# Optimization experiments

Hardware: AMD Instinct MI355X
Metric: run time of the kernel (lower is better)

The kernel has to match this reference:

```python
import jax, jax.numpy as jnp
import numpy as np

RADIUS = 8
EPS = 0.0001


def box_filter_1d(x, axis, r):
    # cumsum summed-area trick; zero padding at edges (matches torch version)
    cs = jnp.swapaxes(jnp.cumsum(x, axis=axis), axis, 0)
    out = jnp.concatenate([
        cs[r:2 * r + 1],
        cs[2 * r + 1:] - cs[:-2 * r - 1],
        cs[-1:] - cs[-2 * r - 1:-r - 1],
    ], axis=0)
    return jnp.swapaxes(out, 0, axis)


def box_filter(x, r):
    for ax in range(2, x.ndim):
        x = box_filter_1d(x, ax, r)
    return x


def setup_inputs() -> dict:
    key = jax.random.key(0)
    k1, k2 = jax.random.split(key)
    I = jax.random.normal(k1, (8, 4, 768, 768), dtype=jnp.float32)
    p = jax.random.uniform(k2, (8, 1, 768, 768), dtype=jnp.float32)
    return {"I": I, "p": p}


def reference(I, p):
    r = RADIUS
    bs, c, h, w = I.shape
    f = lambda t: box_filter(t, r)

    N = f(jnp.ones_like(I[:, :1]))              # (b,1,h,w) window pixel counts
    I_mean = f(I) / N                            # (b,c,h,w)
    p_mean = f(p) / N                            # (b,1,h,w)
    Ip_mean = f(p * I) / N                       # (b,c,h,w)
    first_term = Ip_mean - p_mean * I_mean       # (b,c,h,w)

    # per-pixel cxc covariance of the guide
    cov = jnp.einsum('bchw,bdhw->bcdhw', I, I).reshape(bs, c * c, h, w)
    cov = (f(cov) / N).reshape(bs, c, c, h, w).transpose(0, 3, 4, 1, 2)  # (b,h,w,c,c)
    eps_mat = EPS * jnp.eye(c, dtype=I.dtype)
    second_term = jnp.linalg.inv(cov + eps_mat)  # batched small-matrix inverse

    # NOTE: einsum strings reproduce the original module exactly
    A = jnp.einsum('bchw,bhwcd->bchw', first_term, second_term)
    b = p_mean - jnp.einsum('bchw,bdhw->bhw', A, I_mean)[:, None]  # (b,1,h,w)

    A_mean = f(A) / N
    b_mean = f(b) / N
    q = jnp.einsum('bchw,bdhw->bhw', A_mean, I)[:, None] + b_mean
    return q
```

## Files before the change

### kernel.cpp

```cpp
#include <hip/hip_runtime.h>


#define HH 768
#define WW 768
#define CC 4
#define BB 8
#define RR 8
#define EPSF 1.0e-4f

#define TA 128
#define OUTA 112
#define SHA 24
#define NSTRIPE (HH / SHA)
#define NBAND 7

__device__ __forceinline__ void loadpix(const float* __restrict__ Ib,
                                        const float* __restrict__ pb,
                                        int row, int gc, float pr[19]) {
  const int off = row * WW + gc;
  const int chs = HH * WW;
  float i0 = Ib[off];
  float i1 = Ib[chs + off];
  float i2 = Ib[2 * chs + off];
  float i3 = Ib[3 * chs + off];
  float pv = pb[off];
  pr[0] = i0; pr[1] = i1; pr[2] = i2; pr[3] = i3;
  pr[4] = pv;
  pr[5] = pv * i0; pr[6] = pv * i1; pr[7] = pv * i2; pr[8] = pv * i3;
  pr[9]  = i0 * i0; pr[10] = i0 * i1; pr[11] = i0 * i2; pr[12] = i0 * i3;
  pr[13] = i1 * i1; pr[14] = i1 * i2; pr[15] = i1 * i3;
  pr[16] = i2 * i2; pr[17] = i2 * i3;
  pr[18] = i3 * i3;
}

__global__ __launch_bounds__(TA) void gf_stageA(const float* __restrict__ I,
                                                const float* __restrict__ p,
                                                float2* __restrict__ AB,
                                                float* __restrict__ sumI_ws,
                                                int storeSum) {
  __shared__ float v[TA][20];
  __shared__ float s4[TA][20];
  const int tid = threadIdx.x;
  const int band0 = (int)blockIdx.x * OUTA;
  const int r0 = (int)blockIdx.y * SHA;
  const int batch = (int)blockIdx.z;
  const int gc = band0 - RR + tid;
  const bool colok = (gc >= 0 && gc < WW);

  const float* Ib = I + (size_t)batch * CC * HH * WW;
  const float* pb = p + (size_t)batch * HH * WW;
  float* sIb = sumI_ws + (size_t)batch * HH * WW;

  float s[20];
#pragma unroll
  for (int k = 0; k < 20; ++k) s[k] = 0.0f;

  if (colok) {
    int rlo = r0 - RR - 1; if (rlo < 0) rlo = 0;
    for (int row = rlo; row < r0 + RR; ++row) {
      float pr[19]; loadpix(Ib, pb, row, gc, pr);
#pragma unroll
      for (int k = 0; k < 19; ++k) s[k] += pr[k];
      if (storeSum && r0 == 0)
        sIb[row * WW + gc] = pr[0] + pr[1] + pr[2] + pr[3];
    }
  }

  const int oc = band0 + tid;
  const bool outok = (tid < OUTA) && (oc < WW);
  const int nw = min(oc + RR, WW - 1) - max(oc - RR, 0) + 1;

  for (int r = r0; r < r0 + SHA; ++r) {
    if (colok) {
      int rl = r + RR;
      if (rl < HH) {
        float pr[19]; loadpix(Ib, pb, rl, gc, pr);
#pragma unroll
        for (int k = 0; k < 19; ++k) s[k] += pr[k];
        if (storeSum)
          sIb[rl * WW + gc] = pr[0] + pr[1] + pr[2] + pr[3];
      }
      int rt = r - RR - 1;
      if (rt >= 0) {
        float pr[19]; loadpix(Ib, pb, rt, gc, pr);
#pragma unroll
        for (int k = 0; k < 19; ++k) s[k] -= pr[k];
      }
    }
    {
      float4* vp = (float4*)(&v[tid][0]);
      vp[0] = make_float4(s[0],  s[1],  s[2],  s[3]);
      vp[1] = make_float4(s[4],  s[5],  s[6],  s[7]);
      vp[2] = make_float4(s[8],  s[9],  s[10], s[11]);
      vp[3] = make_float4(s[12], s[13], s[14], s[15]);
      vp[4] = make_float4(s[16], s[17], s[18], 0.0f);
    }
    __syncthreads();
    float t4[20];
    if (tid < TA - 3) {
      const float* a1 = &v[tid + 1][0];
      const float* a2 = &v[tid + 2][0];
      const float* a3 = &v[tid + 3][0];
      float4* op = (float4*)(&s4[tid][0]);
#pragma unroll
      for (int j = 0; j < 5; ++j) {
        float4 xa = ((const float4*)a1)[j];
        float4 xb = ((const float4*)a2)[j];
        float4 xc = ((const float4*)a3)[j];
        float o0 = s[4*j + 0] + xa.x + xb.x + xc.x;
        float o1 = s[4*j + 1] + xa.y + xb.y + xc.y;
        float o2 = s[4*j + 2] + xa.z + xb.z + xc.z;
        float o3 = s[4*j + 3] + xa.w + xb.w + xc.w;
        op[j] = make_float4(o0, o1, o2, o3);
        t4[4*j + 0] = o0; t4[4*j + 1] = o1; t4[4*j + 2] = o2; t4[4*j + 3] = o3;
      }
    }
    __syncthreads();
    if (outok) {
      float h[20];
      const float* q4  = &s4[tid + 4][0];
      const float* q8  = &s4[tid + 8][0];
      const float* q12 = &s4[tid + 12][0];
      const float* q16 = &v[tid + 16][0];
#pragma unroll
      for (int j = 0; j < 5; ++j) {
        float4 a4 = ((const float4*)q4)[j];
        float4 b4 = ((const float4*)q8)[j];
        float4 c4 = ((const float4*)q12)[j];
        float4 d4 = ((const float4*)q16)[j];
        h[4*j + 0] = t4[4*j + 0] + a4.x + b4.x + c4.x + d4.x;
        h[4*j + 1] = t4[4*j + 1] + a4.y + b4.y + c4.y + d4.y;
        h[4*j + 2] = t4[4*j + 2] + a4.z + b4.z + c4.z + d4.z;
        h[4*j + 3] = t4[4*j + 3] + a4.w + b4.w + c4.w + d4.w;
      }
      const int nh = min(r + RR, HH - 1) - max(r - RR, 0) + 1;
      const float invN = 1.0f / (float)(nh * nw);
      float Im0 = h[0] * invN, Im1 = h[1] * invN, Im2 = h[2] * invN, Im3 = h[3] * invN;
      float pm = h[4] * invN;
      float ft0 = h[5] * invN - pm * Im0;
      float ft1 = h[6] * invN - pm * Im1;
      float ft2 = h[7] * invN - pm * Im2;
      float ft3 = h[8] * invN - pm * Im3;
      float m[4][4];
      m[0][0] = h[9]  * invN + EPSF;
      m[0][1] = h[10] * invN;
      m[0][2] = h[11] * invN;
      m[0][3] = h[12] * invN;
      m[1][1] = h[13] * invN + EPSF;
      m[1][2] = h[14] * invN;
      m[1][3] = h[15] * invN;
      m[2][2] = h[16] * invN + EPSF;
      m[2][3] = h[17] * invN;
      m[3][3] = h[18] * invN + EPSF;
      m[1][0] = m[0][1]; m[2][0] = m[0][2]; m[3][0] = m[0][3];
      m[2][1] = m[1][2]; m[3][1] = m[1][3]; m[3][2] = m[2][3];
      float y[4] = {1.0f, 1.0f, 1.0f, 1.0f};
#pragma unroll
      for (int k = 0; k < 4; ++k) {
        float piv = 1.0f / m[k][k];
#pragma unroll
        for (int j = 0; j < 4; ++j) m[k][j] *= piv;
        y[k] *= piv;
#pragma unroll
        for (int i = 0; i < 4; ++i) {
          if (i == k) continue;
          float f = m[i][k];
#pragma unroll
          for (int j = 0; j < 4; ++j) m[i][j] -= f * m[k][j];
          y[i] -= f * y[k];
        }
      }
      float Asum = ft0 * y[0] + ft1 * y[1] + ft2 * y[2] + ft3 * y[3];
      float bv = pm - Asum * (Im0 + Im1 + Im2 + Im3);
      AB[((size_t)batch * HH + r) * WW + oc] = make_float2(Asum, bv);
    }
    __syncthreads();
  }
}

__global__ __launch_bounds__(TA) void gf_stageB(const float* __restrict__ I,
                                                const float2* __restrict__ AB,
                                                const float* __restrict__ sumI_ws,
                                                float* __restrict__ q, int useSum) {
  __shared__ float2 v2[TA];
  __shared__ float2 s42[TA];
  const int tid = threadIdx.x;
  const int band0 = (int)blockIdx.x * OUTA;
  const int r0 = (int)blockIdx.y * SHA;
  const int batch = (int)blockIdx.z;
  const int gc = band0 - RR + tid;
  const bool colok = (gc >= 0 && gc < WW);

  const float2* ABb = AB + (size_t)batch * HH * WW;
  const float* sIb = sumI_ws + (size_t)batch * HH * WW;
  const float* Ib = I + (size_t)batch * CC * HH * WW;

  float sA = 0.0f, sB = 0.0f;
  if (colok) {
    int rlo = r0 - RR - 1; if (rlo < 0) rlo = 0;
    for (int row = rlo; row < r0 + RR; ++row) {
      float2 t = ABb[row * WW + gc];
      sA += t.x; sB += t.y;
    }
  }
  const int oc = band0 + tid;
  const bool outok = (tid < OUTA) && (oc < WW);
  const int nw = min(oc + RR, WW - 1) - max(oc - RR, 0) + 1;

  for (int r = r0; r < r0 + SHA; ++r) {
    if (colok) {
      int rl = r + RR;
      if (rl < HH) { float2 t = ABb[rl * WW + gc]; sA += t.x; sB += t.y; }
      int rt = r - RR - 1;
      if (rt >= 0) { float2 t = ABb[rt * WW + gc]; sA -= t.x; sB -= t.y; }
    }
    v2[tid] = make_float2(sA, sB);
    __syncthreads();
    float tx = 0.0f, ty = 0.0f;
    if (tid < TA - 3) {
      float2 a = v2[tid + 1], b = v2[tid + 2], c = v2[tid + 3];
      tx = sA + a.x + b.x + c.x;
      ty = sB + a.y + b.y + c.y;
      s42[tid] = make_float2(tx, ty);
    }
    __syncthreads();
    if (outok) {
      float2 a = s42[tid + 4], b = s42[tid + 8], c = s42[tid + 12], d = v2[tid + 16];
      float hA = tx + a.x + b.x + c.x + d.x;
      float hB = ty + a.y + b.y + c.y + d.y;
      const int nh = min(r + RR, HH - 1) - max(r - RR, 0) + 1;
      const float invN = 1.0f / (float)(nh * nw);
      const int off = r * WW + oc;
      float sumI;
      if (useSum) {
        sumI = sIb[off];
      } else {
        const int chs = HH * WW;
        sumI = Ib[off] + Ib[chs + off] + Ib[2 * chs + off] + Ib[3 * chs + off];
      }
      q[((size_t)batch * HH + r) * WW + oc] = (hA * sumI + hB) * invN;
    }
    __syncthreads();
  }
}

extern "C" void kernel_launch(void* const* d_in, const int* in_sizes, int n_in,
                              void* d_out, int out_size, void* d_ws, size_t ws_size,
                              hipStream_t stream) {
  const float* I = (const float*)d_in[0];
  const float* p = (const float*)d_in[1];
  float* q = (float*)d_out;

  const size_t npix = (size_t)BB * HH * WW;
  float2* AB = (float2*)d_ws;
  float* sumI_ws = (float*)(AB + npix);
  const size_t need = npix * sizeof(float2) + npix * sizeof(float);
  const int useSum = (ws_size >= need) ? 1 : 0;

  dim3 grid(NBAND, NSTRIPE, BB);
  dim3 block(TA);
  hipLaunchKernelGGL(gf_stageA, grid, block, 0, stream, I, p, AB, sumI_ws, useSum);
  hipLaunchKernelGGL(gf_stageB, grid, block, 0, stream, I, AB, sumI_ws, q, useSum);
}
```

Baseline: 235.6 us.

## Prefetch next rows in stage A and preload sliding window in stage B

Stage A now loads the raw 5 values for the next entering and leaving rows one iteration ahead (software pipelining), computing the 19 products from registers so global latency overlaps the solve. Its stripe height drops from 24 to 16 rows, giving more blocks but more halo recomputation. Stage B, which keeps its own 24-row stripe, loads the whole 41-row window of A/b values and the sumI values into registers up front, removing dependent loads from the per-row loop. This raises register pressure and may reduce occupancy.

```diff
diff --git a/kernel.cpp b/kernel.cpp
--- a/kernel.cpp
+++ b/kernel.cpp
@@ -10,27 +10,33 @@
 
 #define TA 128
 #define OUTA 112
-#define SHA 24
+#define SHA 16
 #define NSTRIPE (HH / SHA)
 #define NBAND 7
 
-__device__ __forceinline__ void loadpix(const float* __restrict__ Ib,
-                                        const float* __restrict__ pb,
-                                        int row, int gc, float pr[19]) {
+#define SHB 24
+#define NSTRIPEB (HH / SHB)
+
+__device__ __forceinline__ void load5(const float* __restrict__ Ib,
+                                      const float* __restrict__ pb,
+                                      int row, int gc, float o[5]) {
   const int off = row * WW + gc;
   const int chs = HH * WW;
-  float i0 = Ib[off];
-  float i1 = Ib[chs + off];
-  float i2 = Ib[2 * chs + off];
-  float i3 = Ib[3 * chs + off];
-  float pv = pb[off];
-  pr[0] = i0; pr[1] = i1; pr[2] = i2; pr[3] = i3;
-  pr[4] = pv;
-  pr[5] = pv * i0; pr[6] = pv * i1; pr[7] = pv * i2; pr[8] = pv * i3;
-  pr[9]  = i0 * i0; pr[10] = i0 * i1; pr[11] = i0 * i2; pr[12] = i0 * i3;
-  pr[13] = i1 * i1; pr[14] = i1 * i2; pr[15] = i1 * i3;
-  pr[16] = i2 * i2; pr[17] = i2 * i3;
-  pr[18] = i3 * i3;
+  o[0] = Ib[off];
+  o[1] = Ib[chs + off];
+  o[2] = Ib[2 * chs + off];
+  o[3] = Ib[3 * chs + off];
+  o[4] = pb[off];
+}
+
+__device__ __forceinline__ void prod19(const float o[5], float pr[19]) {
+  pr[0] = o[0]; pr[1] = o[1]; pr[2] = o[2]; pr[3] = o[3];
+  pr[4] = o[4];
+  pr[5] = o[4] * o[0]; pr[6] = o[4] * o[1]; pr[7] = o[4] * o[2]; pr[8] = o[4] * o[3];
+  pr[9]  = o[0] * o[0]; pr[10] = o[0] * o[1]; pr[11] = o[0] * o[2]; pr[12] = o[0] * o[3];
+  pr[13] = o[1] * o[1]; pr[14] = o[1] * o[2]; pr[15] = o[1] * o[3];
+  pr[16] = o[2] * o[2]; pr[17] = o[2] * o[3];
+  pr[18] = o[3] * o[3];
 }
 
 __global__ __launch_bounds__(TA) void gf_stageA(const float* __restrict__ I,
@@ -58,12 +64,19 @@
   if (colok) {
     int rlo = r0 - RR - 1; if (rlo < 0) rlo = 0;
     for (int row = rlo; row < r0 + RR; ++row) {
-      float pr[19]; loadpix(Ib, pb, row, gc, pr);
+      float o[5]; load5(Ib, pb, row, gc, o);
+      float pr[19]; prod19(o, pr);
 #pragma unroll
       for (int k = 0; k < 19; ++k) s[k] += pr[k];
       if (storeSum && r0 == 0)
-        sIb[row * WW + gc] = pr[0] + pr[1] + pr[2] + pr[3];
-    }
+        sIb[row * WW + gc] = o[0] + o[1] + o[2] + o[3];
+    }
+  }
+
+  float ca[5] = {0,0,0,0,0}, cb[5] = {0,0,0,0,0};
+  if (colok) {
+    load5(Ib, pb, r0 + RR, gc, ca);
+    if (r0 - RR - 1 >= 0) load5(Ib, pb, r0 - RR - 1, gc, cb);
   }
 
   const int oc = band0 + tid;
@@ -71,21 +84,17 @@
   const int nw = min(oc + RR, WW - 1) - max(oc - RR, 0) + 1;
 
   for (int r = r0; r < r0 + SHA; ++r) {
+    float na[5] = {0,0,0,0,0}, nb[5] = {0,0,0,0,0};
     if (colok) {
-      int rl = r + RR;
-      if (rl < HH) {
-        float pr[19]; loadpix(Ib, pb, rl, gc, pr);
-#pragma unroll
-        for (int k = 0; k < 19; ++k) s[k] += pr[k];
-        if (storeSum)
-          sIb[rl * WW + gc] = pr[0] + pr[1] + pr[2] + pr[3];
-      }
-      int rt = r - RR - 1;
-      if (rt >= 0) {
-        float pr[19]; loadpix(Ib, pb, rt, gc, pr);
-#pragma unroll
-        for (int k = 0; k < 19; ++k) s[k] -= pr[k];
-      }
+      float pra[19], prb[19];
+      prod19(ca, pra);
+      prod19(cb, prb);
+#pragma unroll
+      for (int k = 0; k < 19; ++k) s[k] += pra[k] - prb[k];
+      if (storeSum && (r + RR < HH))
+        sIb[(r + RR) * WW + gc] = ca[0] + ca[1] + ca[2] + ca[3];
+      if (r + RR + 1 < HH) load5(Ib, pb, r + RR + 1, gc, na);
+      if (r - RR >= 0)     load5(Ib, pb, r - RR, gc, nb);
     }
     {
       float4* vp = (float4*)(&v[tid][0]);
@@ -175,6 +184,8 @@
       AB[((size_t)batch * HH + r) * WW + oc] = make_float2(Asum, bv);
     }
     __syncthreads();
+#pragma unroll
+    for (int k = 0; k < 5; ++k) { ca[k] = na[k]; cb[k] = nb[k]; }
   }
 }
 
@@ -186,7 +197,7 @@
   __shared__ float2 s42[TA];
   const int tid = threadIdx.x;
   const int band0 = (int)blockIdx.x * OUTA;
-  const int r0 = (int)blockIdx.y * SHA;
+  const int r0 = (int)blockIdx.y * SHB;
   const int batch = (int)blockIdx.z;
   const int gc = band0 - RR + tid;
   const bool colok = (gc >= 0 && gc < WW);
@@ -195,25 +206,33 @@
   const float* sIb = sumI_ws + (size_t)batch * HH * WW;
   const float* Ib = I + (size_t)batch * CC * HH * WW;
 
-  float sA = 0.0f, sB = 0.0f;
-  if (colok) {
-    int rlo = r0 - RR - 1; if (rlo < 0) rlo = 0;
-    for (int row = rlo; row < r0 + RR; ++row) {
-      float2 t = ABb[row * WW + gc];
-      sA += t.x; sB += t.y;
-    }
-  }
   const int oc = band0 + tid;
   const bool outok = (tid < OUTA) && (oc < WW);
   const int nw = min(oc + RR, WW - 1) - max(oc - RR, 0) + 1;
 
-  for (int r = r0; r < r0 + SHA; ++r) {
-    if (colok) {
-      int rl = r + RR;
-      if (rl < HH) { float2 t = ABb[rl * WW + gc]; sA += t.x; sB += t.y; }
-      int rt = r - RR - 1;
-      if (rt >= 0) { float2 t = ABb[rt * WW + gc]; sA -= t.x; sB -= t.y; }
-    }
+  float2 w[SHB + 17];
+#pragma unroll
+  for (int k = 0; k < SHB + 17; ++k) {
+    const int row = r0 - RR - 1 + k;
+    const bool ok = colok && (row >= 0) && (row < HH);
+    w[k] = ok ? ABb[row * WW + gc] : make_float2(0.0f, 0.0f);
+  }
+  float sm[SHB];
+  if (useSum) {
+#pragma unroll
+    for (int j = 0; j < SHB; ++j)
+      sm[j] = outok ? sIb[(r0 + j) * WW + oc] : 0.0f;
+  }
+
+  float sA = 0.0f, sB = 0.0f;
+#pragma unroll
+  for (int k = 0; k < 17; ++k) { sA += w[k].x; sB += w[k].y; }
+
+#pragma unroll
+  for (int j = 0; j < SHB; ++j) {
+    const int r = r0 + j;
+    sA += w[j + 17].x - w[j].x;
+    sB += w[j + 17].y - w[j].y;
     v2[tid] = make_float2(sA, sB);
     __syncthreads();
     float tx = 0.0f, ty = 0.0f;
@@ -230,11 +249,11 @@
       float hB = ty + a.y + b.y + c.y + d.y;
       const int nh = min(r + RR, HH - 1) - max(r - RR, 0) + 1;
       const float invN = 1.0f / (float)(nh * nw);
-      const int off = r * WW + oc;
       float sumI;
       if (useSum) {
-        sumI = sIb[off];
+        sumI = sm[j];
       } else {
+        const int off = r * WW + oc;
         const int chs = HH * WW;
         sumI = Ib[off] + Ib[chs + off] + Ib[2 * chs + off] + Ib[3 * chs + off];
       }
@@ -257,8 +276,9 @@
   const size_t need = npix * sizeof(float2) + npix * sizeof(float);
   const int useSum = (ws_size >= need) ? 1 : 0;
 
-  dim3 grid(NBAND, NSTRIPE, BB);
+  dim3 gridA(NBAND, NSTRIPE, BB);
+  dim3 gridB(NBAND, NSTRIPEB, BB);
   dim3 block(TA);
-  hipLaunchKernelGGL(gf_stageA, grid, block, 0, stream, I, p, AB, sumI_ws, useSum);
-  hipLaunchKernelGGL(gf_stageB, grid, block, 0, stream, I, AB, sumI_ws, q, useSum);
-}
+  hipLaunchKernelGGL(gf_stageA, gridA, block, 0, stream, I, p, AB, sumI_ws, useSum);
+  hipLaunchKernelGGL(gf_stageB, gridB, block, 0, stream, I, AB, sumI_ws, q, useSum);
+}
```

Result: slower. 276.1 us (+17.2%).

## Rewrite stage B horizontal box sum with wavefront shuffles instead of LDS

Applied to the files above, without the earlier changes.

Stage B now assigns one 64-lane wavefront per 48-column by 32-row unit, with four independent units per 256-thread block. The horizontal 17-wide sum uses __shfl_down in place of shared memory and block-wide barriers. This is meant to remove the per-row __syncthreads and LDS traffic. In exchange, the halo overhead per column rises (64 columns loaded for 48 outputs, against 128 for 112 before) and more stripe-initialisation rows are re-read.

```diff
diff --git a/kernel.cpp b/kernel.cpp
--- a/kernel.cpp
+++ b/kernel.cpp
@@ -13,6 +13,13 @@
 #define SHA 24
 #define NSTRIPE (HH / SHA)
 #define NBAND 7
+
+#define OBW 48
+#define NBANDB (WW / OBW)
+#define SHBR 32
+#define NSTRIPB (HH / SHBR)
+#define UNITS (NBANDB * NSTRIPB * BB)
+#define TBB 256
 
 __device__ __forceinline__ void loadpix(const float* __restrict__ Ib,
                                         const float* __restrict__ pb,
@@ -178,69 +185,65 @@
   }
 }
 
-__global__ __launch_bounds__(TA) void gf_stageB(const float* __restrict__ I,
-                                                const float2* __restrict__ AB,
-                                                const float* __restrict__ sumI_ws,
-                                                float* __restrict__ q, int useSum) {
-  __shared__ float2 v2[TA];
-  __shared__ float2 s42[TA];
-  const int tid = threadIdx.x;
-  const int band0 = (int)blockIdx.x * OUTA;
-  const int r0 = (int)blockIdx.y * SHA;
-  const int batch = (int)blockIdx.z;
-  const int gc = band0 - RR + tid;
-  const bool colok = (gc >= 0 && gc < WW);
+__global__ __launch_bounds__(TBB) void gf_stageB(const float* __restrict__ I,
+                                                 const float2* __restrict__ AB,
+                                                 const float* __restrict__ sumI_ws,
+                                                 float* __restrict__ q, int useSum) {
+  const int lane = threadIdx.x & 63;
+  const int wid  = threadIdx.x >> 6;
+  const int unit = (int)blockIdx.x * 4 + wid;
+  const int band   = unit & (NBANDB - 1);
+  const int stripe = (unit >> 4) % NSTRIPB;
+  const int batch  = unit / (NBANDB * NSTRIPB);
+  const int band0 = band * OBW;
+  const int r0 = stripe * SHBR;
 
   const float2* ABb = AB + (size_t)batch * HH * WW;
   const float* sIb = sumI_ws + (size_t)batch * HH * WW;
   const float* Ib = I + (size_t)batch * CC * HH * WW;
 
+  const int gc = band0 - RR + lane;
+  const bool colok = (gc >= 0 && gc < WW);
+  const int oc = band0 + lane;
+  const bool outok = (lane < OBW);
+  const int nw = min(oc + RR, WW - 1) - max(oc - RR, 0) + 1;
+
   float sA = 0.0f, sB = 0.0f;
-  if (colok) {
+  {
     int rlo = r0 - RR - 1; if (rlo < 0) rlo = 0;
     for (int row = rlo; row < r0 + RR; ++row) {
-      float2 t = ABb[row * WW + gc];
-      sA += t.x; sB += t.y;
-    }
-  }
-  const int oc = band0 + tid;
-  const bool outok = (tid < OUTA) && (oc < WW);
-  const int nw = min(oc + RR, WW - 1) - max(oc - RR, 0) + 1;
-
-  for (int r = r0; r < r0 + SHA; ++r) {
+      if (colok) { float2 t = ABb[row * WW + gc]; sA += t.x; sB += t.y; }
+    }
+  }
+
+  for (int r = r0; r < r0 + SHBR; ++r) {
     if (colok) {
       int rl = r + RR;
       if (rl < HH) { float2 t = ABb[rl * WW + gc]; sA += t.x; sB += t.y; }
       int rt = r - RR - 1;
-      if (rt >= 0) { float2 t = ABb[rt * WW + gc]; sA -= t.x; sB -= t.y; }
-    }
-    v2[tid] = make_float2(sA, sB);
-    __syncthreads();
-    float tx = 0.0f, ty = 0.0f;
-    if (tid < TA - 3) {
-      float2 a = v2[tid + 1], b = v2[tid + 2], c = v2[tid + 3];
-      tx = sA + a.x + b.x + c.x;
-      ty = sB + a.y + b.y + c.y;
-      s42[tid] = make_float2(tx, ty);
-    }
-    __syncthreads();
+      if (rt >= 0)  { float2 t = ABb[rt * WW + gc]; sA -= t.x; sB -= t.y; }
+    }
+    float a1 = __shfl_down(sA, 1), a2 = __shfl_down(sA, 2), a3 = __shfl_down(sA, 3);
+    float b1 = __shfl_down(sB, 1), b2 = __shfl_down(sB, 2), b3 = __shfl_down(sB, 3);
+    float s4A = sA + a1 + a2 + a3;
+    float s4B = sB + b1 + b2 + b3;
+    float hA = s4A + __shfl_down(s4A, 4) + __shfl_down(s4A, 8) + __shfl_down(s4A, 12)
+             + __shfl_down(sA, 16);
+    float hB = s4B + __shfl_down(s4B, 4) + __shfl_down(s4B, 8) + __shfl_down(s4B, 12)
+             + __shfl_down(sB, 16);
     if (outok) {
-      float2 a = s42[tid + 4], b = s42[tid + 8], c = s42[tid + 12], d = v2[tid + 16];
-      float hA = tx + a.x + b.x + c.x + d.x;
-      float hB = ty + a.y + b.y + c.y + d.y;
       const int nh = min(r + RR, HH - 1) - max(r - RR, 0) + 1;
       const float invN = 1.0f / (float)(nh * nw);
-      const int off = r * WW + oc;
       float sumI;
       if (useSum) {
-        sumI = sIb[off];
+        sumI = sIb[r * WW + oc];
       } else {
+        const int off = r * WW + oc;
         const int chs = HH * WW;
         sumI = Ib[off] + Ib[chs + off] + Ib[2 * chs + off] + Ib[3 * chs + off];
       }
       q[((size_t)batch * HH + r) * WW + oc] = (hA * sumI + hB) * invN;
     }
-    __syncthreads();
   }
 }
 
@@ -257,8 +260,10 @@
   const size_t need = npix * sizeof(float2) + npix * sizeof(float);
   const int useSum = (ws_size >= need) ? 1 : 0;
 
-  dim3 grid(NBAND, NSTRIPE, BB);
-  dim3 block(TA);
-  hipLaunchKernelGGL(gf_stageA, grid, block, 0, stream, I, p, AB, sumI_ws, useSum);
-  hipLaunchKernelGGL(gf_stageB, grid, block, 0, stream, I, AB, sumI_ws, q, useSum);
-}
+  dim3 gridA(NBAND, NSTRIPE, BB);
+  dim3 gridB(UNITS / 4, 1, 1);
+  dim3 blockA(TA);
+  dim3 blockB(TBB);
+  hipLaunchKernelGGL(gf_stageA, gridA, blockA, 0, stream, I, p, AB, sumI_ws, useSum);
+  hipLaunchKernelGGL(gf_stageB, gridB, blockB, 0, stream, I, AB, sumI_ws, q, useSum);
+}
```

Result: slower. 242.1 us (+2.7%).
